# Optimization experiments

Measured on AMD Instinct MI355X. Metric: run time of the kernel, lower is better.

Reference implementation:

```python
import jax, jax.numpy as jnp
import numpy as np
import math

MODEL_DIM = 4096
NUM_EXPERTS = 64
NUM_TOKENS = 8192
CAPACITY_FACTOR = 1.0
MIN_CAPACITY = 4


def setup_inputs() -> dict:
    key = jax.random.key(0)
    k1, k2, k3 = jax.random.split(key, 3)
    x = jax.random.normal(k1, (NUM_TOKENS, MODEL_DIM), dtype=jnp.float32)
    wg_weight = jax.random.normal(k2, (NUM_EXPERTS, MODEL_DIM), dtype=jnp.float32) * (1.0 / math.sqrt(MODEL_DIM))
    uniform_noise = jax.random.uniform(k3, (NUM_TOKENS, NUM_EXPERTS), dtype=jnp.float32)
    return {"x": x, "wg_weight": wg_weight, "uniform_noise": uniform_noise}


def reference(x, wg_weight, uniform_noise):
    # gate projection in fp32 (torch module forces .float())
    logits = jnp.einsum('sd,ed->se', x.astype(jnp.float32), wg_weight.astype(jnp.float32))
    gates = jax.nn.softmax(logits, axis=1)  # [s, e]
    s, e = gates.shape
    capacity = max(math.ceil(s / e * CAPACITY_FACTOR), MIN_CAPACITY)  # static: 128

    indices1_s = jnp.argmax(gates, axis=1)                      # [s]
    mask1 = jax.nn.one_hot(indices1_s, e, dtype=jnp.int32)      # [s, e]
    exp_counts = jnp.sum(mask1, axis=0)                         # [e]

    # load-balancing aux loss
    me = jnp.mean(gates, axis=0)
    ce = jnp.mean(mask1.astype(jnp.float32), axis=0)
    l_aux = jnp.sum(me * ce) * e

    # random capacity selection: per-expert top-`capacity` tokens by uniform noise
    mask1_rand = mask1.astype(jnp.float32) * uniform_noise      # [s, e]
    _, top_idx = jax.lax.top_k(mask1_rand.T, capacity)          # [e, capacity] token ids
    sel = jnp.zeros((s, e), jnp.int32).at[top_idx, jnp.arange(e)[:, None]].set(1)
    new_mask1 = mask1 * sel                                     # [s, e]

    # capacity-slot assignment via cumsum
    locations1 = jnp.cumsum(new_mask1, axis=0) - 1              # [s, e]
    locations1_s = jnp.sum(locations1 * new_mask1, axis=1)      # [s]

    gates_masked = gates * new_mask1.astype(jnp.float32)        # [s, e]
    locations1_sc = jax.nn.one_hot(locations1_s, capacity, dtype=jnp.float32)  # [s, c]
    combine_weights = jnp.einsum('se,sc->sec', gates_masked, locations1_sc)     # [s, e, c]
    dispatch_mask = combine_weights.astype(bool)
    return l_aux, combine_weights, dispatch_mask, exp_counts
```

## Files before the change

### kernel.cpp

```cpp
#include <hip/hip_runtime.h>

#define S    8192
#define Dm   4096
#define E    64
#define CAP  128
#define CCH  32
#define KC   (Dm/CCH)
#define KSUB 16
#define XSTR 260
#define WSTR 68

#define CW_OFF 1
#define DM_OFF (1 + (size_t)S*E*CAP)
#define EC_OFF (1 + 2*(size_t)S*E*CAP)
#define OUT_BYTES ((1 + 2*(size_t)S*E*CAP + E) * sizeof(float))
#define K1B_BLOCKS 512

__global__ __launch_bounds__(256)
void k1_partial(const float* __restrict__ x, const float* __restrict__ wg,
                float* __restrict__ part) {
    __shared__ float xs[KSUB][XSTR];
    __shared__ float wsh[KSUB][WSTR];
    const int tb  = blockIdx.x >> 5;
    const int c   = blockIdx.x & 31;
    const int tid = threadIdx.x;
    const int tt  = tid & 31;
    const int ee  = tid >> 5;
    const int k0  = c * KC;

    float acc[64];
    #pragma unroll
    for (int i = 0; i < 64; i++) acc[i] = 0.f;

    const int xr = tid >> 2;
    const int xc = tid & 3;
    const int we = tid >> 2;
    const int wk = (tid & 3) * 4;

    for (int su = 0; su < KC / KSUB; su++) {
        const int ks0 = k0 + su * KSUB;
        #pragma unroll
        for (int i = 0; i < 4; i++) {
            const int row = i * 64 + xr;
            const float4 v = *(const float4*)(x + (size_t)(tb*256 + row) * Dm + ks0 + xc*4);
            xs[xc*4+0][row] = v.x;
            xs[xc*4+1][row] = v.y;
            xs[xc*4+2][row] = v.z;
            xs[xc*4+3][row] = v.w;
        }
        {
            const float4 v = *(const float4*)(wg + (size_t)we * Dm + ks0 + wk);
            wsh[wk+0][we] = v.x; wsh[wk+1][we] = v.y;
            wsh[wk+2][we] = v.z; wsh[wk+3][we] = v.w;
        }
        __syncthreads();
        #pragma unroll 8
        for (int kk = 0; kk < KSUB; kk++) {
            const float4 a0 = *(const float4*)&xs[kk][tt*4];
            const float4 a1 = *(const float4*)&xs[kk][128 + tt*4];
            const float4 w0 = *(const float4*)&wsh[kk][ee*8];
            const float4 w1 = *(const float4*)&wsh[kk][ee*8+4];
            const float av[8] = {a0.x,a0.y,a0.z,a0.w,a1.x,a1.y,a1.z,a1.w};
            const float wv[8] = {w0.x,w0.y,w0.z,w0.w,w1.x,w1.y,w1.z,w1.w};
            #pragma unroll
            for (int t = 0; t < 8; t++)
                #pragma unroll
                for (int e = 0; e < 8; e++)
                    acc[t*8+e] = fmaf(av[t], wv[e], acc[t*8+e]);
        }
        __syncthreads();
    }
    #pragma unroll
    for (int t = 0; t < 8; t++) {
        const int token = (t < 4) ? (tt*4 + t) : (128 + tt*4 + (t - 4));
        float* dst = part + ((size_t)c * S + tb*256 + token) * E + ee*8;
        *(float4*)(dst)     = make_float4(acc[t*8+0], acc[t*8+1], acc[t*8+2], acc[t*8+3]);
        *(float4*)(dst + 4) = make_float4(acc[t*8+4], acc[t*8+5], acc[t*8+6], acc[t*8+7]);
    }
}

__global__ __launch_bounds__(256, 1)
void k1b_softmax(const float* __restrict__ part, float* __restrict__ gate_val,
                 int* __restrict__ idx1, int* __restrict__ counts,
                 float* __restrict__ me_part) {
    const int tid = threadIdx.x, wv = tid >> 6, ln = tid & 63;
    float me_loc = 0.f;
    #pragma unroll
    for (int t = 0; t < 4; t++) {
        const int token = blockIdx.x * 16 + wv * 4 + t;
        float p = 0.f;
        #pragma unroll
        for (int c = 0; c < CCH; c++) p += part[((size_t)c * S + token) * E + ln];
        float v = p; int i = ln;
        #pragma unroll
        for (int off = 1; off < 64; off <<= 1) {
            float ov = __shfl_xor(v, off, 64);
            int   oi = __shfl_xor(i, off, 64);
            if (ov > v || (ov == v && oi < i)) { v = ov; i = oi; }
        }
        float g = __expf(p - v);
        float ssum = g;
        #pragma unroll
        for (int off = 1; off < 64; off <<= 1) ssum += __shfl_xor(ssum, off, 64);
        me_loc += g / ssum;
        if (ln == 0) {
            gate_val[token] = 1.0f / ssum;
            idx1[token] = i;
            atomicAdd(&counts[i], 1);
        }
    }
    __shared__ float gs[4][64];
    gs[wv][ln] = me_loc;
    __syncthreads();
    if (tid < 64)
        me_part[(size_t)blockIdx.x * 64 + tid] = gs[0][tid] + gs[1][tid] + gs[2][tid] + gs[3][tid];
}

__device__ __forceinline__ int block_reduce_sum(int v, int* tmp4, int tid) {
    #pragma unroll
    for (int off = 1; off < 64; off <<= 1) v += __shfl_xor(v, off, 64);
    __syncthreads();
    if ((tid & 63) == 0) tmp4[tid >> 6] = v;
    __syncthreads();
    return tmp4[0] + tmp4[1] + tmp4[2] + tmp4[3];
}

__device__ __forceinline__ int block_scan_incl(int val, int* a, int* b, int tid, int* total) {
    __syncthreads();
    a[tid] = val;
    __syncthreads();
    int* src = a; int* dst = b;
    #pragma unroll
    for (int off = 1; off < 256; off <<= 1) {
        int v = src[tid];
        if (tid >= off) v += src[tid - off];
        dst[tid] = v;
        __syncthreads();
        int* t = src; src = dst; dst = t;
    }
    *total = src[255];
    return src[tid];
}

__global__ __launch_bounds__(256, 1)
void k2_select(const int* __restrict__ idx1, const float* __restrict__ gate_val,
               const float* __restrict__ noise, const int* __restrict__ counts,
               const float* __restrict__ me_part, float* __restrict__ out) {
    const int e = blockIdx.x;
    const int tid = threadIdx.x;
    __shared__ int idx_s[S];
    __shared__ unsigned short l_tok[S];
    __shared__ float l_ns[S];
    __shared__ int sa[256], sb[256];
    __shared__ int tmp4[4];

    for (int i = tid; i < S; i += 256) idx_s[i] = idx1[i];
    __syncthreads();

    int cnt = 0;
    #pragma unroll
    for (int j4 = 0; j4 < 8; j4++) {
        const int4 q = *(const int4*)&idx_s[tid * 32 + j4 * 4];
        cnt += (q.x == e) + (q.y == e) + (q.z == e) + (q.w == e);
    }
    int total_n;
    int incl = block_scan_incl(cnt, sa, sb, tid, &total_n);
    int pos = incl - cnt;
    const int n = total_n;
    #pragma unroll
    for (int j4 = 0; j4 < 8; j4++) {
        const int4 q = *(const int4*)&idx_s[tid * 32 + j4 * 4];
        const int qv[4] = {q.x, q.y, q.z, q.w};
        #pragma unroll
        for (int u = 0; u < 4; u++) {
            const int s = tid * 32 + j4 * 4 + u;
            if (qv[u] == e) {
                l_tok[pos] = (unsigned short)s;
                l_ns[pos]  = noise[(size_t)s * E + e];
                pos++;
            }
        }
    }
    __syncthreads();

    if (tid == 0) out[EC_OFF + e] = (float)n;

    unsigned int V = 0u;
    if (n > CAP) {
        unsigned int lo = 0u, hi = 0x3F800000u;
        while (hi - lo > 1u) {
            const unsigned int mid = (lo + hi) >> 1;
            int c = 0;
            for (int i2 = tid; i2 < n; i2 += 256)
                c += (__float_as_uint(l_ns[i2]) >= mid);
            const int cge = block_reduce_sum(c, tmp4, tid);
            if (cge >= CAP) lo = mid; else hi = mid;
        }
        V = lo;
    }

    const int m = (n + 255) >> 8;
    const int i_begin = min(n, tid * m);
    const int i_end   = min(n, i_begin + m);
    int gt_l = 0, eq_l = 0;
    for (int i2 = i_begin; i2 < i_end; i2++) {
        const unsigned int b = __float_as_uint(l_ns[i2]);
        gt_l += (b > V); eq_l += (b == V);
    }
    int tot_gt, tot_eq;
    const int incl_gt = block_scan_incl(gt_l, sa, sb, tid, &tot_gt);
    (void)incl_gt;
    const int incl_eq = block_scan_incl(eq_l, sa, sb, tid, &tot_eq);
    const int eq_excl = incl_eq - eq_l;
    const int take_eq = CAP - tot_gt;
    const int sel_l = gt_l + max(0, min(eq_l, take_eq - eq_excl));
    int tot_sel;
    const int incl_sel = block_scan_incl(sel_l, sa, sb, tid, &tot_sel);
    int slot = incl_sel - sel_l;
    int eq_seen = eq_excl;
    for (int i2 = i_begin; i2 < i_end; i2++) {
        const unsigned int b = __float_as_uint(l_ns[i2]);
        bool sel;
        if (b > V) sel = true;
        else if (b == V) { sel = (eq_seen < take_eq); eq_seen++; }
        else sel = false;
        if (sel) {
            const int tok = l_tok[i2];
            const float g = gate_val[tok];
            const size_t off = (size_t)tok * (E * CAP) + (size_t)e * CAP + slot;
            out[CW_OFF + off] = g;
            out[DM_OFF + off] = 1.0f;
            slot++;
        }
    }

    if (e == 0 && tid < 64) {
        float ms = 0.f;
        for (int b2 = 0; b2 < K1B_BLOCKS; b2++) ms += me_part[(size_t)b2 * 64 + tid];
        float la = (ms / (float)S) * ((float)counts[tid] / (float)S);
        #pragma unroll
        for (int off = 1; off < 64; off <<= 1) la += __shfl_xor(la, off, 64);
        if (tid == 0) out[0] = la * (float)E;
    }
}

extern "C" void kernel_launch(void* const* d_in, const int* in_sizes, int n_in,
                              void* d_out, int out_size, void* d_ws, size_t ws_size,
                              hipStream_t stream) {
    const float* x     = (const float*)d_in[0];
    const float* wg    = (const float*)d_in[1];
    const float* noise = (const float*)d_in[2];
    float* out = (float*)d_out;
    float* ws  = (float*)d_ws;

    float* gate_val = ws;
    int*   idx1     = (int*)(ws + 8192);
    int*   counts   = (int*)(ws + 16384);
    float* me_part  = ws + 16448;
    float* part     = ws + 49216;

    (void)hipMemsetAsync(counts, 0, 64 * sizeof(int), stream);
    (void)hipMemsetAsync(out, 0, OUT_BYTES, stream);
    k1_partial  <<<dim3(1024),       dim3(256), 0, stream>>>(x, wg, part);
    k1b_softmax <<<dim3(K1B_BLOCKS), dim3(256), 0, stream>>>(part, gate_val, idx1, counts, me_part);
    k2_select   <<<dim3(E),          dim3(256), 0, stream>>>(idx1, gate_val, noise, counts, me_part, out);
}
```

Baseline: 712.9 us.

## Fuse output zeroing into GEMM kernel and transpose partial-sum layout

```diff
diff --git a/kernel.cpp b/kernel.cpp
--- a/kernel.cpp
+++ b/kernel.cpp
@@ -13,17 +13,35 @@
 #define CW_OFF 1
 #define DM_OFF (1 + (size_t)S*E*CAP)
 #define EC_OFF (1 + 2*(size_t)S*E*CAP)
-#define OUT_BYTES ((1 + 2*(size_t)S*E*CAP + E) * sizeof(float))
-#define K1B_BLOCKS 512
+#define ZERO_MAIN (2*(size_t)S*E*CAP)
+#define K1B_BLOCKS 1024
+
+typedef float f32x4 __attribute__((ext_vector_type(4)));
 
 __global__ __launch_bounds__(256)
 void k1_partial(const float* __restrict__ x, const float* __restrict__ wg,
-                float* __restrict__ part) {
+                float* __restrict__ part, float* __restrict__ out) {
+    const int bid = blockIdx.x;
+    const int tid = threadIdx.x;
+    const int r3  = bid % 3;
+
+    if (r3 == 1) {
+        const int zid = bid / 3;
+        f32x4* zb = (f32x4*)(out + (size_t)zid * 262144);
+        const f32x4 z4 = {0.f, 0.f, 0.f, 0.f};
+        #pragma unroll 8
+        for (int i = tid; i < 65536; i += 256)
+            __builtin_nontemporal_store(z4, zb + i);
+        if (zid == 0 && tid < 65)
+            __builtin_nontemporal_store(0.f, out + ZERO_MAIN + tid);
+        return;
+    }
+
     __shared__ float xs[KSUB][XSTR];
     __shared__ float wsh[KSUB][WSTR];
-    const int tb  = blockIdx.x >> 5;
-    const int c   = blockIdx.x & 31;
-    const int tid = threadIdx.x;
+    const int gid = (bid / 3) * 2 + (r3 >> 1);
+    const int tb  = gid >> 5;
+    const int c   = gid & 31;
     const int tt  = tid & 31;
     const int ee  = tid >> 5;
     const int k0  = c * KC;
@@ -73,7 +91,7 @@
     #pragma unroll
     for (int t = 0; t < 8; t++) {
         const int token = (t < 4) ? (tt*4 + t) : (128 + tt*4 + (t - 4));
-        float* dst = part + ((size_t)c * S + tb*256 + token) * E + ee*8;
+        float* dst = part + ((size_t)(tb*256 + token) * CCH + c) * E + ee*8;
         *(float4*)(dst)     = make_float4(acc[t*8+0], acc[t*8+1], acc[t*8+2], acc[t*8+3]);
         *(float4*)(dst + 4) = make_float4(acc[t*8+4], acc[t*8+5], acc[t*8+6], acc[t*8+7]);
     }
@@ -84,36 +102,61 @@
                  int* __restrict__ idx1, int* __restrict__ counts,
                  float* __restrict__ me_part) {
     const int tid = threadIdx.x, wv = tid >> 6, ln = tid & 63;
-    float me_loc = 0.f;
-    #pragma unroll
-    for (int t = 0; t < 4; t++) {
-        const int token = blockIdx.x * 16 + wv * 4 + t;
-        float p = 0.f;
-        #pragma unroll
-        for (int c = 0; c < CCH; c++) p += part[((size_t)c * S + token) * E + ln];
-        float v = p; int i = ln;
-        #pragma unroll
-        for (int off = 1; off < 64; off <<= 1) {
-            float ov = __shfl_xor(v, off, 64);
-            int   oi = __shfl_xor(i, off, 64);
-            if (ov > v || (ov == v && oi < i)) { v = ov; i = oi; }
-        }
-        float g = __expf(p - v);
-        float ssum = g;
-        #pragma unroll
-        for (int off = 1; off < 64; off <<= 1) ssum += __shfl_xor(ssum, off, 64);
-        me_loc += g / ssum;
+    const int er = ln & 15;
+    __shared__ float gs[4][64];
+    float me4[4] = {0.f, 0.f, 0.f, 0.f};
+
+    #pragma unroll
+    for (int t = 0; t < 2; t++) {
+        const int token = (blockIdx.x * 4 + wv) * 2 + t;
+        const float* tp = part + (size_t)token * (CCH * E);
+        float4 a[8];
+        #pragma unroll
+        for (int i = 0; i < 8; i++)
+            a[i] = *(const float4*)(tp + i * 256 + ln * 4);
+        float4 s = a[0];
+        #pragma unroll
+        for (int i = 1; i < 8; i++) { s.x += a[i].x; s.y += a[i].y; s.z += a[i].z; s.w += a[i].w; }
+        #pragma unroll
+        for (int mask = 16; mask <= 32; mask <<= 1) {
+            s.x += __shfl_xor(s.x, mask, 64);
+            s.y += __shfl_xor(s.y, mask, 64);
+            s.z += __shfl_xor(s.z, mask, 64);
+            s.w += __shfl_xor(s.w, mask, 64);
+        }
+        float m = fmaxf(fmaxf(s.x, s.y), fmaxf(s.z, s.w));
+        #pragma unroll
+        for (int mask = 1; mask <= 8; mask <<= 1) m = fmaxf(m, __shfl_xor(m, mask, 64));
+        const float e0 = __expf(s.x - m), e1 = __expf(s.y - m),
+                    e2 = __expf(s.z - m), e3 = __expf(s.w - m);
+        float ss = ((e0 + e1) + (e2 + e3));
+        #pragma unroll
+        for (int mask = 1; mask <= 8; mask <<= 1) ss += __shfl_xor(ss, mask, 64);
+        float bv = s.x; int bi = er * 4;
+        if (s.y > bv) { bv = s.y; bi = er * 4 + 1; }
+        if (s.z > bv) { bv = s.z; bi = er * 4 + 2; }
+        if (s.w > bv) { bv = s.w; bi = er * 4 + 3; }
+        #pragma unroll
+        for (int mask = 1; mask <= 8; mask <<= 1) {
+            const float ov = __shfl_xor(bv, mask, 64);
+            const int   oi = __shfl_xor(bi, mask, 64);
+            if (ov > bv || (ov == bv && oi < bi)) { bv = ov; bi = oi; }
+        }
+        const float inv = 1.f / ss;
         if (ln == 0) {
-            gate_val[token] = 1.0f / ssum;
-            idx1[token] = i;
-            atomicAdd(&counts[i], 1);
-        }
-    }
-    __shared__ float gs[4][64];
-    gs[wv][ln] = me_loc;
+            gate_val[token] = inv;
+            idx1[token] = bi;
+            atomicAdd(&counts[bi], 1);
+        }
+        me4[0] += e0 * inv; me4[1] += e1 * inv; me4[2] += e2 * inv; me4[3] += e3 * inv;
+    }
+    if (ln < 16) {
+        gs[wv][er*4+0] = me4[0]; gs[wv][er*4+1] = me4[1];
+        gs[wv][er*4+2] = me4[2]; gs[wv][er*4+3] = me4[3];
+    }
     __syncthreads();
     if (tid < 64)
-        me_part[(size_t)blockIdx.x * 64 + tid] = gs[0][tid] + gs[1][tid] + gs[2][tid] + gs[3][tid];
+        me_part[(size_t)blockIdx.x * 64 + tid] = (gs[0][tid] + gs[1][tid]) + (gs[2][tid] + gs[3][tid]);
 }
 
 __device__ __forceinline__ int block_reduce_sum(int v, int* tmp4, int tid) {
@@ -257,11 +300,10 @@
     int*   idx1     = (int*)(ws + 8192);
     int*   counts   = (int*)(ws + 16384);
     float* me_part  = ws + 16448;
-    float* part     = ws + 49216;
+    float* part     = ws + 81984;
 
     (void)hipMemsetAsync(counts, 0, 64 * sizeof(int), stream);
-    (void)hipMemsetAsync(out, 0, OUT_BYTES, stream);
-    k1_partial  <<<dim3(1024),       dim3(256), 0, stream>>>(x, wg, part);
+    k1_partial  <<<dim3(1536),       dim3(256), 0, stream>>>(x, wg, part, out);
     k1b_softmax <<<dim3(K1B_BLOCKS), dim3(256), 0, stream>>>(part, gate_val, idx1, counts, me_part);
     k2_select   <<<dim3(E),          dim3(256), 0, stream>>>(idx1, gate_val, noise, counts, me_part, out);
 }
```

Result: slower. 753.3 us (+5.7%).
